# Kernel optimization log

Hardware: AMD Instinct MI355X
Metric: run time of the kernel (lower is better)

The kernel has to match this reference:

```python
import jax, jax.numpy as jnp
import numpy as np

D = 128          # state_dim
N_RBF = 20       # n radial basis functions
R_CUT = 10.0
N_NODES = 20000
N_EDGES = 320000
N_GRAPHS = 64
N_ATOMS = 10
ROUNDS = 2       # num_message_passing_rounds


def silu(x):
    return x * jax.nn.sigmoid(x)


def setup_inputs() -> dict:
    key = jax.random.key(0)
    ks = jax.random.split(key, 16)

    def p(k, shape, scale=None):
        scale = (1.0 / np.sqrt(shape[0])) if scale is None else scale
        return (jax.random.normal(k, shape, jnp.float32) * scale).astype(jnp.float32)

    return {
        "edge_src": jax.random.randint(ks[0], (N_EDGES,), 0, N_NODES, jnp.int32),
        "edge_dst": jax.random.randint(ks[1], (N_EDGES,), 0, N_NODES, jnp.int32),
        "edge_vec": jax.random.normal(ks[2], (N_EDGES, 3), jnp.float32) * 2.0,
        "atom_types": jax.random.randint(ks[3], (N_NODES,), 0, N_ATOMS, jnp.int32),
        "node_graph_index": jnp.sort(jax.random.randint(ks[4], (N_NODES,), 0, N_GRAPHS, jnp.int32)),
        "embedding": p(ks[5], (N_ATOMS, D), 1.0),
        "phi_w1": p(ks[6], (D, D)), "phi_b1": jnp.zeros((D,), jnp.float32),
        "phi_w2": p(ks[7], (D, 3 * D)), "phi_b2": jnp.zeros((3 * D,), jnp.float32),
        "filt_w": p(ks[8], (N_RBF, 3 * D)), "filt_b": jnp.zeros((3 * D,), jnp.float32),
        "upd_w1": p(ks[9], (2 * D, D)), "upd_b1": jnp.zeros((D,), jnp.float32),
        "upd_w2": p(ks[10], (D, 3 * D)), "upd_b2": jnp.zeros((3 * D,), jnp.float32),
        "U_w": p(ks[11], (D, D)), "V_w": p(ks[12], (D, D)),
        "out_w1": p(ks[13], (D, D)), "out_b1": jnp.zeros((D,), jnp.float32),
        "out_w2": p(ks[14], (D, 1)), "out_b2": jnp.zeros((1,), jnp.float32),
    }


def reference(edge_src, edge_dst, edge_vec, atom_types, node_graph_index,
              embedding, phi_w1, phi_b1, phi_w2, phi_b2, filt_w, filt_b,
              upd_w1, upd_b1, upd_w2, upd_b2, U_w, V_w,
              out_w1, out_b1, out_w2, out_b2):
    # init scalar states from atom-type embedding; vector states zero
    s = embedding[atom_types]                       # [N, D]
    v = jnp.zeros((N_NODES, 3, D), s.dtype)         # [N, 3, D]

    # geometry (constant across rounds)
    r = jnp.linalg.norm(edge_vec, axis=1)           # [E]
    k = jnp.arange(1, N_RBF + 1, dtype=s.dtype)
    rbf = jnp.sin(k[None, :] * jnp.pi * r[:, None] / R_CUT) / r[:, None]   # [E, n]
    fcut = 0.5 * (jnp.cos(jnp.pi * r / R_CUT) + 1.0) * (r < R_CUT)         # [E]
    W = (rbf @ filt_w + filt_b) * fcut[:, None]     # [E, 3D] filter * cosine cutoff
    dirs = edge_vec / r[:, None]                    # [E, 3] unit edge vectors

    for _ in range(ROUNDS):
        # ---- message block ----
        phi = silu(s[edge_src] @ phi_w1 + phi_b1) @ phi_w2 + phi_b2        # [E, 3D]
        m = phi * W
        m1, m2, m3 = m[:, :D], m[:, D:2 * D], m[:, 2 * D:]
        dv = v[edge_src] * m1[:, None, :] + dirs[:, :, None] * m3[:, None, :]  # [E, 3, D]
        s = s + jax.ops.segment_sum(m2, edge_dst, num_segments=N_NODES)
        v = v + jax.ops.segment_sum(dv, edge_dst, num_segments=N_NODES)

        # ---- update block ----
        U = v @ U_w                                  # [N, 3, D]
        Vp = v @ V_w                                 # [N, 3, D]
        UV = jnp.sum(U * Vp, axis=1)                 # [N, D]
        Vn = jnp.linalg.norm(Vp, axis=1)             # [N, D]
        a = silu(jnp.concatenate([Vn, s], axis=1) @ upd_w1 + upd_b1) @ upd_w2 + upd_b2  # [N, 3D]
        avv, asv, ass = a[:, :D], a[:, D:2 * D], a[:, 2 * D:]
        s = s + ass + UV * asv
        v = v + U * avv[:, None, :]

    # graph readout: index_add over node_graph_index, then output MLP
    g = jax.ops.segment_sum(s, node_graph_index, num_segments=N_GRAPHS)    # [G, D]
    return (silu(g @ out_w1 + out_b1) @ out_w2 + out_b2).reshape(-1)       # [G]
```

## Files before the change

### kernel.cpp

```cpp
#include <hip/hip_runtime.h>

#define NN 20000
#define NE 320000
#define NG 64
#define D 128
#define D3 384
#define NRBF 20
#define RBF_ROW 24
#define PI_F 3.14159265358979323846f
#define RCUT 10.0f

typedef unsigned int uint;
typedef unsigned short ushort;
typedef __attribute__((ext_vector_type(8))) short bf16x8;
typedef __attribute__((ext_vector_type(4))) float f32x4;

__device__ __forceinline__ float silu_f(float x) {
    return x / (1.0f + __expf(-x));
}
__device__ __forceinline__ float b2f(ushort u) {
    return __uint_as_float(((uint)u) << 16);
}
__device__ __forceinline__ ushort f2b(float f) {
    uint u = __float_as_uint(f);
    u = u + 0x7fffu + ((u >> 16) & 1u);
    return (ushort)(u >> 16);
}
__device__ __forceinline__ float plo(uint u) { return __uint_as_float(u << 16); }
__device__ __forceinline__ float phi_(uint u) { return __uint_as_float(u & 0xffff0000u); }

#define MFMA3(acc, aH, aL, bH, bL)                                          \
    acc = __builtin_amdgcn_mfma_f32_16x16x32_bf16(aL, bH, acc, 0, 0, 0);    \
    acc = __builtin_amdgcn_mfma_f32_16x16x32_bf16(aH, bL, acc, 0, 0, 0);    \
    acc = __builtin_amdgcn_mfma_f32_16x16x32_bf16(aH, bH, acc, 0, 0, 0);

__global__ __launch_bounds__(256) void mega_init(
    float* __restrict__ g, int* __restrict__ deg,
    const float* __restrict__ pw1, const float* __restrict__ pw2,
    ushort* __restrict__ w1th, ushort* __restrict__ w1tl,
    ushort* __restrict__ w2th, ushort* __restrict__ w2tl,
    const float* __restrict__ Uw, const float* __restrict__ Vw,
    const float* __restrict__ uw1, const float* __restrict__ uw2,
    ushort* __restrict__ uwt, ushort* __restrict__ vwt,
    ushort* __restrict__ u1t, ushort* __restrict__ u2t)
{
    int stride = gridDim.x * blockDim.x;
    int idx0 = blockIdx.x * blockDim.x + threadIdx.x;
    for (int i = idx0; i < NG * D; i += stride) g[i] = 0.f;
    for (int i = idx0; i < NN; i += stride) deg[i] = 0;
    for (int i = idx0; i < D * D; i += stride) {
        int j = i >> 7, k = i & 127;
        float x = pw1[k * D + j]; ushort h = f2b(x);
        w1th[i] = h; w1tl[i] = f2b(x - b2f(h));
        float a = Uw[k * D + j]; ushort ha = f2b(a);
        uwt[i] = ha; uwt[D * D + i] = f2b(a - b2f(ha));
        float b = Vw[k * D + j]; ushort hb = f2b(b);
        vwt[i] = hb; vwt[D * D + i] = f2b(b - b2f(hb));
    }
    for (int i = idx0; i < D3 * D; i += stride) {
        int j = i >> 7, k = i & 127;
        float x = pw2[k * D3 + j]; ushort h = f2b(x);
        w2th[i] = h; w2tl[i] = f2b(x - b2f(h));
        float y = uw2[k * D3 + j]; ushort hy = f2b(y);
        u2t[i] = hy; u2t[D3 * D + i] = f2b(y - b2f(hy));
    }
    for (int i = idx0; i < 2 * D * D; i += stride) {
        int j = i >> 8, k = i & 255;
        float x = uw1[k * D + j]; ushort h = f2b(x);
        u1t[i] = h; u1t[2 * D * D + i] = f2b(x - b2f(h));
    }
}

__global__ __launch_bounds__(256) void csr_count(
    const int* __restrict__ dst, int* __restrict__ deg)
{
    int e = blockIdx.x * blockDim.x + threadIdx.x;
    if (e < NE) atomicAdd(&deg[dst[e]], 1);
}

__global__ __launch_bounds__(1024) void scan_all(
    const int* __restrict__ deg, int* __restrict__ offs,
    int* __restrict__ cursor, int* __restrict__ bpos)
{
    __shared__ int part[1024];
    __shared__ int bc[64];
    int t = threadIdx.x;
    if (t < 64) bc[t] = 0;
    __syncthreads();
    const int per = (NN + 1023) / 1024;
    int base = t * per;
    int sum = 0;
    for (int i = 0; i < per; i++) {
        int idx = base + i;
        if (idx < NN) {
            int dg = deg[idx];
            sum += dg;
            int b = dg > 63 ? 63 : dg;
            atomicAdd(&bc[b], 1);
        }
    }
    part[t] = sum;
    __syncthreads();
    for (int off = 1; off < 1024; off <<= 1) {
        int vv = (t >= off) ? part[t - off] : 0;
        __syncthreads();
        part[t] += vv;
        __syncthreads();
    }
    int run = part[t] - sum;
    for (int i = 0; i < per; i++) {
        int idx = base + i;
        if (idx < NN) {
            offs[idx] = run;
            cursor[idx] = run;
            run += deg[idx];
        }
    }
    if (t == 1023) offs[NN] = run;
    __syncthreads();
    if (t == 0) {
        int r2 = 0;
        for (int b = 63; b >= 0; b--) { bpos[b] = r2; r2 += bc[b]; }
    }
}

__global__ __launch_bounds__(256) void scatter_all(
    const int* __restrict__ dst, int* __restrict__ cursor, int* __restrict__ eid,
    const int* __restrict__ deg, int* __restrict__ bpos, int* __restrict__ perm)
{
    int i = blockIdx.x * blockDim.x + threadIdx.x;
    if (i < NE) {
        int p = atomicAdd(&cursor[dst[i]], 1);
        eid[p] = i;
    }
    if (i < NN) {
        int b = deg[i]; if (b > 63) b = 63;
        int p = atomicAdd(&bpos[b], 1);
        perm[p] = i;
    }
}

__global__ __launch_bounds__(256) void edge_geom(
    const float* __restrict__ evec,
    float* __restrict__ rbf, float4* __restrict__ geo)
{
    int e = blockIdx.x * blockDim.x + threadIdx.x;
    if (e >= NE) return;
    float x = evec[e * 3 + 0], y = evec[e * 3 + 1], z = evec[e * 3 + 2];
    float r = sqrtf(x * x + y * y + z * z);
    float inv = 1.0f / r;
    float f = (r < RCUT) ? 0.5f * (cosf(PI_F * r / RCUT) + 1.0f) : 0.0f;
    float4 g;
    g.x = x * inv; g.y = y * inv; g.z = z * inv; g.w = f;
    geo[e] = g;
    float base = PI_F * r / RCUT;
    float sf = inv * f;
    #pragma unroll
    for (int k = 0; k < NRBF; k++) {
        rbf[(size_t)e * RBF_ROW + k] = sinf((float)(k + 1) * base) * sf;
    }
}

__global__ __launch_bounds__(128) void phi10(
    const float* __restrict__ emb,
    const float* __restrict__ w1, const float* __restrict__ b1,
    const float* __restrict__ w2, const float* __restrict__ b2,
    uint* __restrict__ ptab)
{
    __shared__ float el[D];
    __shared__ float hl[D];
    int t = blockIdx.x, j = threadIdx.x;
    el[j] = emb[t * D + j];
    __syncthreads();
    float acc = b1[j];
    for (int k = 0; k < D; k++) acc += el[k] * w1[k * D + j];
    hl[j] = silu_f(acc);
    __syncthreads();
    float a1 = b2[D + j], a2 = b2[2 * D + j];
    for (int k = 0; k < D; k++) {
        float h = hl[k];
        a1 += h * w2[k * D3 + D + j];
        a2 += h * w2[k * D3 + 2 * D + j];
    }
    ptab[t * D + j] = (uint)f2b(a1) | ((uint)f2b(a2) << 16);
}

__global__ __launch_bounds__(512)
__attribute__((amdgpu_waves_per_eu(4, 4)))
void node_gather_r0(
    const int* __restrict__ eid, const int* __restrict__ offs,
    const int* __restrict__ perm, const int* __restrict__ src,
    const int* __restrict__ atype, const float* __restrict__ emb,
    const uint* __restrict__ ptab,
    const float* __restrict__ rbf, const float4* __restrict__ geo,
    const float* __restrict__ filt_w, const float* __restrict__ filt_b,
    float* __restrict__ s_new, float* __restrict__ v_new)
{
    int wave = threadIdx.x >> 6;
    int lane = threadIdx.x & 63;
    int widx = blockIdx.x * 4 + (wave >> 1);
    if (widx >= NN) return;
    int node = __builtin_amdgcn_readfirstlane(perm[widx]);
    int half = wave & 1;
    int d = half * 64 + lane;

    float wr1[NRBF], wr2[NRBF];
    #pragma unroll
    for (int k = 0; k < NRBF; k++) {
        wr1[k] = filt_w[k * D3 + D + d];
        wr2[k] = filt_w[k * D3 + 2 * D + d];
    }
    float fb1 = filt_b[D + d], fb2 = filt_b[2 * D + d];
    int e0 = __builtin_amdgcn_readfirstlane(offs[node]);
    int e1 = __builtin_amdgcn_readfirstlane(offs[node + 1]);

    float acc_s = 0.f, av0 = 0.f, av1 = 0.f, av2 = 0.f;

    for (int i = e0; i < e1; i += 2) {
        bool hb = (i + 1 < e1);
        int ea = __builtin_amdgcn_readfirstlane(eid[i]);
        int eb = __builtin_amdgcn_readfirstlane(eid[hb ? i + 1 : i]);
        float mb = hb ? 1.0f : 0.0f;
        int sa = __builtin_amdgcn_readfirstlane(src[ea]);
        int sb = __builtin_amdgcn_readfirstlane(src[eb]);
        int ta = __builtin_amdgcn_readfirstlane(atype[sa]);
        int tb = __builtin_amdgcn_readfirstlane(atype[sb]);
        float4 ga = geo[ea];
        float4 gb = geo[eb];
        const float* rpa = rbf + (size_t)ea * RBF_ROW;
        const float* rpb = rbf + (size_t)eb * RBF_ROW;
        uint pka = ptab[ta * D + d];
        uint pkb = ptab[tb * D + d];

        float Wa1 = ga.w * fb1, Wa2 = ga.w * fb2;
        float Wb1 = gb.w * fb1, Wb2 = gb.w * fb2;
        #pragma unroll
        for (int k = 0; k < NRBF; k++) {
            float ra = rpa[k], rb = rpb[k];
            Wa1 += ra * wr1[k]; Wa2 += ra * wr2[k];
            Wb1 += rb * wr1[k]; Wb2 += rb * wr2[k];
        }
        float pa1 = plo(pka), pa2 = phi_(pka);
        float pb1 = plo(pkb), pb2 = phi_(pkb);

        float m2a = pa1 * Wa1, m3a = pa2 * Wa2;
        float m2b = pb1 * Wb1 * mb, m3b = pb2 * Wb2 * mb;
        acc_s += m2a + m2b;
        av0 += ga.x * m3a + gb.x * m3b;
        av1 += ga.y * m3a + gb.y * m3b;
        av2 += ga.z * m3a + gb.z * m3b;
    }

    int tn = __builtin_amdgcn_readfirstlane(atype[node]);
    s_new[node * D + d] = emb[tn * D + d] + acc_s;
    v_new[(node * 3 + 0) * D + d] = av0;
    v_new[(node * 3 + 1) * D + d] = av1;
    v_new[(node * 3 + 2) * D + d] = av2;
}

__global__ __launch_bounds__(512)
__attribute__((amdgpu_waves_per_eu(4, 4)))
void node_gather(
    const int* __restrict__ eid, const int* __restrict__ offs,
    const int* __restrict__ perm, const int* __restrict__ src,
    const ushort* __restrict__ pv,
    const float* __restrict__ s_old, const float* __restrict__ v_old,
    const float* __restrict__ rbf, const float4* __restrict__ geo,
    const float* __restrict__ filt_w, const float* __restrict__ filt_b,
    float* __restrict__ s_new, float* __restrict__ v_new)
{
    int wave = threadIdx.x >> 6;
    int lane = threadIdx.x & 63;
    int widx = blockIdx.x * 4 + (wave >> 1);
    if (widx >= NN) return;
    int node = __builtin_amdgcn_readfirstlane(perm[widx]);
    int half = wave & 1;
    int d = half * 64 + lane;

    float wr0[NRBF], wr1[NRBF], wr2[NRBF];
    #pragma unroll
    for (int k = 0; k < NRBF; k++) {
        wr0[k] = filt_w[k * D3 + d];
        wr1[k] = filt_w[k * D3 + D + d];
        wr2[k] = filt_w[k * D3 + 2 * D + d];
    }
    float fb0 = filt_b[d], fb1 = filt_b[D + d], fb2 = filt_b[2 * D + d];
    int e0 = __builtin_amdgcn_readfirstlane(offs[node]);
    int e1 = __builtin_amdgcn_readfirstlane(offs[node + 1]);

    float acc_s = 0.f, av0 = 0.f, av1 = 0.f, av2 = 0.f;
    size_t doff = (size_t)d * 6;

    for (int i = e0; i < e1; i += 2) {
        bool hb = (i + 1 < e1);
        int ea = __builtin_amdgcn_readfirstlane(eid[i]);
        int eb = __builtin_amdgcn_readfirstlane(eid[hb ? i + 1 : i]);
        float mb = hb ? 1.0f : 0.0f;
        int sa = __builtin_amdgcn_readfirstlane(src[ea]);
        int sb = __builtin_amdgcn_readfirstlane(src[eb]);
        float4 ga = geo[ea];
        float4 gb = geo[eb];
        const float* rpa = rbf + (size_t)ea * RBF_ROW;
        const float* rpb = rbf + (size_t)eb * RBF_ROW;
        uint3 pka = *(const uint3*)(pv + (size_t)sa * 768 + doff);
        uint3 pkb = *(const uint3*)(pv + (size_t)sb * 768 + doff);

        float Wa0 = ga.w * fb0, Wa1 = ga.w * fb1, Wa2 = ga.w * fb2;
        float Wb0 = gb.w * fb0, Wb1 = gb.w * fb1, Wb2 = gb.w * fb2;
        #pragma unroll
        for (int k = 0; k < NRBF; k++) {
            float ra = rpa[k], rb = rpb[k];
            Wa0 += ra * wr0[k]; Wa1 += ra * wr1[k]; Wa2 += ra * wr2[k];
            Wb0 += rb * wr0[k]; Wb1 += rb * wr1[k]; Wb2 += rb * wr2[k];
        }
        float pa0 = plo(pka.x), pa1 = phi_(pka.x), pa2 = plo(pka.y);
        float va0 = phi_(pka.y), va1 = plo(pka.z), va2 = phi_(pka.z);
        float pb0 = plo(pkb.x), pb1 = phi_(pkb.x), pb2 = plo(pkb.y);
        float vb0 = phi_(pkb.y), vb1 = plo(pkb.z), vb2 = phi_(pkb.z);

        float m1a = pa0 * Wa0, m2a = pa1 * Wa1, m3a = pa2 * Wa2;
        float m1b = pb0 * Wb0 * mb, m2b = pb1 * Wb1 * mb, m3b = pb2 * Wb2 * mb;
        acc_s += m2a + m2b;
        av0 += va0 * m1a + ga.x * m3a + vb0 * m1b + gb.x * m3b;
        av1 += va1 * m1a + ga.y * m3a + vb1 * m1b + gb.y * m3b;
        av2 += va2 * m1a + ga.z * m3a + vb2 * m1b + gb.z * m3b;
    }

    s_new[node * D + d] = s_old[node * D + d] + acc_s;
    v_new[(node * 3 + 0) * D + d] = v_old[(node * 3 + 0) * D + d] + av0;
    v_new[(node * 3 + 1) * D + d] = v_old[(node * 3 + 1) * D + d] + av1;
    v_new[(node * 3 + 2) * D + d] = v_old[(node * 3 + 2) * D + d] + av2;
}

template<bool FUSE>
__global__ __launch_bounds__(256) void node_vupd_mfma(
    float* __restrict__ s, float* __restrict__ v, ushort* __restrict__ pv,
    const ushort* __restrict__ uwt, const ushort* __restrict__ vwt,
    const ushort* __restrict__ u1t, const ushort* __restrict__ u2t,
    const float* __restrict__ ub1, const float* __restrict__ ub2,
    const ushort* __restrict__ w1th, const ushort* __restrict__ w1tl,
    const float* __restrict__ pb1,
    const ushort* __restrict__ w2th, const ushort* __restrict__ w2tl,
    const float* __restrict__ pb2)
{
    __shared__ __align__(16) char smem[47616];
    ushort* U_lds  = (ushort*)(smem);
    float*  UV_lds = (float*)(smem + 13056);
    ushort* a_hi   = (ushort*)(smem + 21504);
    ushort* a_lo   = a_hi + 48 * 136;
    ushort* x_hi   = (ushort*)(smem + 21504);
    ushort* x_lo   = x_hi + 16 * 264;
    ushort* h_hi   = x_lo + 16 * 264;
    ushort* h_lo   = h_hi + 16 * 136;
    float*  a_out  = (float*)(smem + 21504);

    int tid = threadIdx.x;
    int wave = tid >> 6, lane = tid & 63;
    int arow = lane & 15, kg = lane >> 4;
    int n0 = blockIdx.x * 16;

    #pragma unroll
    for (int it = 0; it < 6; it++) {
        int f4 = it * 256 + tid;
        int row = f4 >> 5;
        int c4 = (f4 & 31) * 4;
        int i = row >> 4, n = row & 15;
        float4 vv = *(const float4*)&v[((size_t)(n0 + n) * 3 + i) * D + c4];
        ushort h0 = f2b(vv.x), h1 = f2b(vv.y), h2 = f2b(vv.z), h3 = f2b(vv.w);
        ushort l0 = f2b(vv.x - b2f(h0)), l1 = f2b(vv.y - b2f(h1));
        ushort l2 = f2b(vv.z - b2f(h2)), l3 = f2b(vv.w - b2f(h3));
        uint2 ph; ph.x = (uint)h0 | ((uint)h1 << 16); ph.y = (uint)h2 | ((uint)h3 << 16);
        uint2 pl; pl.x = (uint)l0 | ((uint)l1 << 16); pl.y = (uint)l2 | ((uint)l3 << 16);
        *(uint2*)&a_hi[row * 136 + c4] = ph;
        *(uint2*)&a_lo[row * 136 + c4] = pl;
    }
    __syncthreads();

    f32x4 accU[3][2], accVp[3][2];
    #pragma unroll
    for (int i = 0; i < 3; i++)
        #pragma unroll
        for (int jtl = 0; jtl < 2; jtl++) {
            accU[i][jtl] = (f32x4){0.f, 0.f, 0.f, 0.f};
            accVp[i][jtl] = (f32x4){0.f, 0.f, 0.f, 0.f};
        }
    #pragma unroll
    for (int i = 0; i < 3; i++) {
        #pragma unroll
        for (int t = 0; t < 4; t++) {
            bf16x8 aH = *(const bf16x8*)&a_hi[(i * 16 + arow) * 136 + t * 32 + kg * 8];
            bf16x8 aL = *(const bf16x8*)&a_lo[(i * 16 + arow) * 136 + t * 32 + kg * 8];
            #pragma unroll
            for (int jtl = 0; jtl < 2; jtl++) {
                int j = (wave * 2 + jtl) * 16 + arow;
                bf16x8 bH = *(const bf16x8*)&uwt[(size_t)j * 128 + t * 32 + kg * 8];
                bf16x8 bL = *(const bf16x8*)&uwt[(size_t)D * D + (size_t)j * 128 + t * 32 + kg * 8];
                MFMA3(accU[i][jtl], aH, aL, bH, bL)
                bf16x8 cH = *(const bf16x8*)&vwt[(size_t)j * 128 + t * 32 + kg * 8];
                bf16x8 cL = *(const bf16x8*)&vwt[(size_t)D * D + (size_t)j * 128 + t * 32 + kg * 8];
                MFMA3(accVp[i][jtl], aH, aL, cH, cL)
            }
        }
    }
    __syncthreads();

    #pragma unroll
    for (int jtl = 0; jtl < 2; jtl++) {
        int jcol = (wave * 2 + jtl) * 16 + arow;
        #pragma unroll
        for (int r = 0; r < 4; r++) {
            int n = kg * 4 + r;
            #pragma unroll
            for (int i = 0; i < 3; i++)
                U_lds[(i * 16 + n) * 136 + jcol] = f2b(accU[i][jtl][r]);
            float uv = accU[0][jtl][r] * accVp[0][jtl][r]
                     + accU[1][jtl][r] * accVp[1][jtl][r]
                     + accU[2][jtl][r] * accVp[2][jtl][r];
            float nn = accVp[0][jtl][r] * accVp[0][jtl][r]
                     + accVp[1][jtl][r] * accVp[1][jtl][r]
                     + accVp[2][jtl][r] * accVp[2][jtl][r];
            UV_lds[n * 132 + jcol] = uv;
            float vn = sqrtf(nn);
            ushort hh = f2b(vn);
            x_hi[n * 264 + jcol] = hh;
            x_lo[n * 264 + jcol] = f2b(vn - b2f(hh));
        }
    }
    for (int it = 0; it < 8; it++) {
        int t8 = it * 256 + tid;
        int n = t8 >> 7, j = t8 & 127;
        float sv = s[(size_t)(n0 + n) * D + j];
        ushort hh = f2b(sv);
        x_hi[n * 264 + 128 + j] = hh;
        x_lo[n * 264 + 128 + j] = f2b(sv - b2f(hh));
    }
    __syncthreads();

    {
        f32x4 acc1[2];
        acc1[0] = (f32x4){0.f, 0.f, 0.f, 0.f};
        acc1[1] = (f32x4){0.f, 0.f, 0.f, 0.f};
        #pragma unroll
        for (int t = 0; t < 8; t++) {
            bf16x8 aH = *(const bf16x8*)&x_hi[arow * 264 + t * 32 + kg * 8];
            bf16x8 aL = *(const bf16x8*)&x_lo[arow * 264 + t * 32 + kg * 8];
            #pragma unroll
            for (int jtl = 0; jtl < 2; jtl++) {
                int j = (wave * 2 + jtl) * 16 + arow;
                bf16x8 bH = *(const bf16x8*)&u1t[(size_t)j * 256 + t * 32 + kg * 8];
                bf16x8 bL = *(const bf16x8*)&u1t[(size_t)2 * D * D + (size_t)j * 256 + t * 32 + kg * 8];
                MFMA3(acc1[jtl], aH, aL, bH, bL)
            }
        }
        #pragma unroll
        for (int jtl = 0; jtl < 2; jtl++) {
            int j = (wave * 2 + jtl) * 16 + arow;
            float bias = ub1[j];
            #pragma unroll
            for (int r = 0; r < 4; r++) {
                int n = kg * 4 + r;
                float hv = silu_f(acc1[jtl][r] + bias);
                ushort hh = f2b(hv);
                h_hi[n * 136 + j] = hh;
                h_lo[n * 136 + j] = f2b(hv - b2f(hh));
            }
        }
    }
    __syncthreads();

    f32x4 acc2[6];
    #pragma unroll
    for (int q = 0; q < 6; q++) acc2[q] = (f32x4){0.f, 0.f, 0.f, 0.f};
    #pragma unroll
    for (int t = 0; t < 4; t++) {
        bf16x8 aH = *(const bf16x8*)&h_hi[arow * 136 + t * 32 + kg * 8];
        bf16x8 aL = *(const bf16x8*)&h_lo[arow * 136 + t * 32 + kg * 8];
        #pragma unroll
        for (int q = 0; q < 6; q++) {
            int j = (wave * 6 + q) * 16 + arow;
            bf16x8 bH = *(const bf16x8*)&u2t[(size_t)j * 128 + t * 32 + kg * 8];
            bf16x8 bL = *(const bf16x8*)&u2t[(size_t)D3 * D + (size_t)j * 128 + t * 32 + kg * 8];
            MFMA3(acc2[q], aH, aL, bH, bL)
        }
    }
    __syncthreads();

    #pragma unroll
    for (int q = 0; q < 6; q++) {
        int j = (wave * 6 + q) * 16 + arow;
        float bias = ub2[j];
        #pragma unroll
        for (int r = 0; r < 4; r++)
            a_out[(kg * 4 + r) * 392 + j] = acc2[q][r] + bias;
    }
    __syncthreads();

    float snew_reg[8];
    #pragma unroll
    for (int it = 0; it < 8; it++) {
        int t8 = it * 256 + tid;
        int n = t8 >> 7, j = t8 & 127;
        float a0 = a_out[n * 392 + j];
        float a1 = a_out[n * 392 + 128 + j];
        float a2 = a_out[n * 392 + 256 + j];
        size_t sidx = (size_t)(n0 + n) * D + j;
        float snew = s[sidx] + a2 + UV_lds[n * 132 + j] * a1;
        s[sidx] = snew;
        snew_reg[it] = snew;
        float vf[3];
        #pragma unroll
        for (int i = 0; i < 3; i++) {
            size_t idx = ((size_t)(n0 + n) * 3 + i) * D + j;
            vf[i] = v[idx] + b2f(U_lds[(i * 16 + n) * 136 + j]) * a0;
            v[idx] = vf[i];
        }
        if (FUSE) {
            ushort* pvp = pv + ((size_t)(n0 + n) * 128 + j) * 6;
            pvp[3] = f2b(vf[0]);
            pvp[4] = f2b(vf[1]);
            pvp[5] = f2b(vf[2]);
        }
    }

    if (!FUSE) return;

    __syncthreads();
    #pragma unroll
    for (int it = 0; it < 8; it++) {
        int t8 = it * 256 + tid;
        int n = t8 >> 7, j = t8 & 127;
        float sv = snew_reg[it];
        ushort hh = f2b(sv);
        x_hi[n * 264 + j] = hh;
        x_lo[n * 264 + j] = f2b(sv - b2f(hh));
    }
    __syncthreads();

    {
        f32x4 accp[2];
        accp[0] = (f32x4){0.f, 0.f, 0.f, 0.f};
        accp[1] = (f32x4){0.f, 0.f, 0.f, 0.f};
        #pragma unroll
        for (int t = 0; t < 4; t++) {
            bf16x8 aH = *(const bf16x8*)&x_hi[arow * 264 + t * 32 + kg * 8];
            bf16x8 aL = *(const bf16x8*)&x_lo[arow * 264 + t * 32 + kg * 8];
            #pragma unroll
            for (int jtl = 0; jtl < 2; jtl++) {
                int j = (wave * 2 + jtl) * 16 + arow;
                bf16x8 bH = *(const bf16x8*)&w1th[(size_t)j * 128 + t * 32 + kg * 8];
                bf16x8 bL = *(const bf16x8*)&w1tl[(size_t)j * 128 + t * 32 + kg * 8];
                MFMA3(accp[jtl], aH, aL, bH, bL)
            }
        }
        __syncthreads();
        #pragma unroll
        for (int jtl = 0; jtl < 2; jtl++) {
            int j = (wave * 2 + jtl) * 16 + arow;
            float bias = pb1[j];
            #pragma unroll
            for (int r = 0; r < 4; r++) {
                int n = kg * 4 + r;
                float hv = silu_f(accp[jtl][r] + bias);
                ushort hh = f2b(hv);
                h_hi[n * 136 + j] = hh;
                h_lo[n * 136 + j] = f2b(hv - b2f(hh));
            }
        }
    }
    __syncthreads();

    {
        f32x4 accq[6];
        #pragma unroll
        for (int q = 0; q < 6; q++) accq[q] = (f32x4){0.f, 0.f, 0.f, 0.f};
        #pragma unroll
        for (int t = 0; t < 4; t++) {
            bf16x8 aH = *(const bf16x8*)&h_hi[arow * 136 + t * 32 + kg * 8];
            bf16x8 aL = *(const bf16x8*)&h_lo[arow * 136 + t * 32 + kg * 8];
            #pragma unroll
            for (int q = 0; q < 6; q++) {
                int j = (wave * 6 + q) * 16 + arow;
                bf16x8 bH = *(const bf16x8*)&w2th[(size_t)j * 128 + t * 32 + kg * 8];
                bf16x8 bL = *(const bf16x8*)&w2tl[(size_t)j * 128 + t * 32 + kg * 8];
                MFMA3(accq[q], aH, aL, bH, bL)
            }
        }
        #pragma unroll
        for (int q = 0; q < 6; q++) {
            int j = (wave * 6 + q) * 16 + arow;
            float bias = pb2[j];
            int seg = j >> 7;
            int ch  = j & 127;
            #pragma unroll
            for (int r = 0; r < 4; r++) {
                pv[((size_t)(n0 + kg * 4 + r) * 128 + ch) * 6 + seg] = f2b(accq[q][r] + bias);
            }
        }
    }
}

__global__ __launch_bounds__(128) void graph_sum(
    const float* __restrict__ s, const int* __restrict__ gi, float* __restrict__ g)
{
    int d = threadIdx.x;
    int n0 = blockIdx.x * 64;
    int n1 = n0 + 64; if (n1 > NN) n1 = NN;
    if (n0 >= NN) return;
    int cur = gi[n0];
    float acc = 0.0f;
    for (int n = n0; n < n1; n++) {
        int gn = gi[n];
        if (gn != cur) { atomicAdd(&g[cur * D + d], acc); acc = 0.0f; cur = gn; }
        acc += s[n * D + d];
    }
    atomicAdd(&g[cur * D + d], acc);
}

__global__ __launch_bounds__(128) void out_mlp(
    const float* __restrict__ g,
    const float* __restrict__ w1, const float* __restrict__ b1,
    const float* __restrict__ w2, const float* __restrict__ b2,
    float* __restrict__ out)
{
    __shared__ float gl[D];
    __shared__ float red[2];
    int j = threadIdx.x;
    int gr = blockIdx.x;
    gl[j] = g[gr * D + j];
    __syncthreads();
    float acc = b1[j];
    for (int k = 0; k < D; k++) acc += gl[k] * w1[k * D + j];
    float h = silu_f(acc) * w2[j];
    #pragma unroll
    for (int off = 32; off >= 1; off >>= 1) h += __shfl_down(h, off);
    if ((j & 63) == 0) red[j >> 6] = h;
    __syncthreads();
    if (j == 0) out[gr] = red[0] + red[1] + b2[0];
}

extern "C" void kernel_launch(void* const* d_in, const int* in_sizes, int n_in,
                              void* d_out, int out_size, void* d_ws, size_t ws_size,
                              hipStream_t stream)
{
    const int*   edge_src   = (const int*)  d_in[0];
    const int*   edge_dst   = (const int*)  d_in[1];
    const float* edge_vec   = (const float*)d_in[2];
    const int*   atom_types = (const int*)  d_in[3];
    const int*   node_gi    = (const int*)  d_in[4];
    const float* embedding  = (const float*)d_in[5];
    const float* phi_w1     = (const float*)d_in[6];
    const float* phi_b1     = (const float*)d_in[7];
    const float* phi_w2     = (const float*)d_in[8];
    const float* phi_b2     = (const float*)d_in[9];
    const float* filt_w     = (const float*)d_in[10];
    const float* filt_b     = (const float*)d_in[11];
    const float* upd_w1     = (const float*)d_in[12];
    const float* upd_b1     = (const float*)d_in[13];
    const float* upd_w2     = (const float*)d_in[14];
    const float* upd_b2     = (const float*)d_in[15];
    const float* U_w        = (const float*)d_in[16];
    const float* V_w        = (const float*)d_in[17];
    const float* out_w1     = (const float*)d_in[18];
    const float* out_b1     = (const float*)d_in[19];
    const float* out_w2     = (const float*)d_in[20];
    const float* out_b2     = (const float*)d_in[21];

    float* ws = (float*)d_ws;
    size_t o = 0;
    float* s_a   = ws + o; o += (size_t)NN * D;
    float* s_b   = ws + o; o += (size_t)NN * D;
    float* v_a   = ws + o; o += (size_t)NN * 3 * D;
    float* v_b   = ws + o; o += (size_t)NN * 3 * D;
    float* pv_f  = ws + o; o += (size_t)NN * 384;
    float* rbf_f = ws + o; o += (size_t)NE * RBF_ROW;
    float* geo   = ws + o; o += (size_t)NE * 4;
    float* g     = ws + o; o += (size_t)NG * D;
    float* w1t_f = ws + o; o += (size_t)D * D;
    float* w2t_f = ws + o; o += (size_t)D3 * D;
    float* uwt_f = ws + o; o += (size_t)D * D;
    float* vwt_f = ws + o; o += (size_t)D * D;
    float* u1t_f = ws + o; o += (size_t)2 * D * D;
    float* u2t_f = ws + o; o += (size_t)D3 * D;
    float* ptab_f= ws + o; o += (size_t)10 * D;
    int* deg     = (int*)(ws + o); o += NN;
    int* offs    = (int*)(ws + o); o += NN + 1;
    int* cursor  = (int*)(ws + o); o += NN;
    int* perm    = (int*)(ws + o); o += NN;
    int* bpos    = (int*)(ws + o); o += 64;
    int* eidb    = (int*)(ws + o); o += NE;

    ushort* pv    = (ushort*)pv_f;
    ushort* w1th  = (ushort*)w1t_f;
    ushort* w1tl  = w1th + (size_t)D * D;
    ushort* w2th  = (ushort*)w2t_f;
    ushort* w2tl  = w2th + (size_t)D3 * D;
    ushort* uwt   = (ushort*)uwt_f;
    ushort* vwt   = (ushort*)vwt_f;
    ushort* u1t   = (ushort*)u1t_f;
    ushort* u2t   = (ushort*)u2t_f;
    uint*   ptab  = (uint*)ptab_f;

    mega_init<<<512, 256, 0, stream>>>(g, deg, phi_w1, phi_w2,
                                       w1th, w1tl, w2th, w2tl,
                                       U_w, V_w, upd_w1, upd_w2,
                                       uwt, vwt, u1t, u2t);
    csr_count<<<(NE + 255) / 256, 256, 0, stream>>>(edge_dst, deg);
    scan_all<<<1, 1024, 0, stream>>>(deg, offs, cursor, bpos);
    scatter_all<<<(NE + 255) / 256, 256, 0, stream>>>(edge_dst, cursor, eidb,
                                                      deg, bpos, perm);
    edge_geom<<<(NE + 255) / 256, 256, 0, stream>>>(edge_vec, rbf_f, (float4*)geo);
    phi10<<<10, 128, 0, stream>>>(embedding, phi_w1, phi_b1, phi_w2, phi_b2, ptab);

    node_gather_r0<<<NN / 4, 512, 0, stream>>>(eidb, offs, perm, edge_src,
                                               atom_types, embedding, ptab,
                                               rbf_f, (const float4*)geo,
                                               filt_w, filt_b, s_b, v_b);
    node_vupd_mfma<true><<<NN / 16, 256, 0, stream>>>(s_b, v_b, pv,
                                                      uwt, vwt, u1t, u2t,
                                                      upd_b1, upd_b2,
                                                      w1th, w1tl, phi_b1,
                                                      w2th, w2tl, phi_b2);
    node_gather<<<NN / 4, 512, 0, stream>>>(eidb, offs, perm, edge_src, pv,
                                            s_b, v_b, rbf_f,
                                            (const float4*)geo, filt_w, filt_b,
                                            s_a, v_a);
    node_vupd_mfma<false><<<NN / 16, 256, 0, stream>>>(s_a, v_a, pv,
                                                       uwt, vwt, u1t, u2t,
                                                       upd_b1, upd_b2,
                                                       w1th, w1tl, phi_b1,
                                                       w2th, w2tl, phi_b2);

    graph_sum<<<(NN + 63) / 64, 128, 0, stream>>>(s_a, node_gi, g);
    out_mlp<<<NG, 128, 0, stream>>>(g, out_w1, out_b1, out_w2, out_b2, (float*)d_out);
}
```

Baseline: 663.4 us.

## Fuse degree count into edge_geom, graph readout into last update, keep U in registers

The edge-degree atomic count moves into the edge geometry kernel, and the separate graph_sum kernel is replaced by per-element atomicAdds into g inside the final node update. The node update now keeps U and UV in MFMA accumulator registers and writes outputs in the accumulator layout, no longer staging them through LDS. This cuts LDS use, which may raise occupancy. The final round also skips writing s and v back to global memory. The costs are many more global atomics on g, with 64 graphs contending, and less coalesced stores.

```diff
diff --git a/kernel.cpp b/kernel.cpp
--- a/kernel.cpp
+++ b/kernel.cpp
@@ -71,13 +71,6 @@
     }
 }
 
-__global__ __launch_bounds__(256) void csr_count(
-    const int* __restrict__ dst, int* __restrict__ deg)
-{
-    int e = blockIdx.x * blockDim.x + threadIdx.x;
-    if (e < NE) atomicAdd(&deg[dst[e]], 1);
-}
-
 __global__ __launch_bounds__(1024) void scan_all(
     const int* __restrict__ deg, int* __restrict__ offs,
     int* __restrict__ cursor, int* __restrict__ bpos)
@@ -140,12 +133,14 @@
     }
 }
 
-__global__ __launch_bounds__(256) void edge_geom(
-    const float* __restrict__ evec,
+__global__ __launch_bounds__(256) void edge_geom_count(
+    const float* __restrict__ evec, const int* __restrict__ dst,
+    int* __restrict__ deg,
     float* __restrict__ rbf, float4* __restrict__ geo)
 {
     int e = blockIdx.x * blockDim.x + threadIdx.x;
     if (e >= NE) return;
+    atomicAdd(&deg[dst[e]], 1);
     float x = evec[e * 3 + 0], y = evec[e * 3 + 1], z = evec[e * 3 + 2];
     float r = sqrtf(x * x + y * y + z * z);
     float inv = 1.0f / r;
@@ -335,6 +330,7 @@
 template<bool FUSE>
 __global__ __launch_bounds__(256) void node_vupd_mfma(
     float* __restrict__ s, float* __restrict__ v, ushort* __restrict__ pv,
+    const int* __restrict__ gi, float* __restrict__ g,
     const ushort* __restrict__ uwt, const ushort* __restrict__ vwt,
     const ushort* __restrict__ u1t, const ushort* __restrict__ u2t,
     const float* __restrict__ ub1, const float* __restrict__ ub2,
@@ -343,16 +339,14 @@
     const ushort* __restrict__ w2th, const ushort* __restrict__ w2tl,
     const float* __restrict__ pb2)
 {
-    __shared__ __align__(16) char smem[47616];
-    ushort* U_lds  = (ushort*)(smem);
-    float*  UV_lds = (float*)(smem + 13056);
-    ushort* a_hi   = (ushort*)(smem + 21504);
-    ushort* a_lo   = a_hi + 48 * 136;
-    ushort* x_hi   = (ushort*)(smem + 21504);
-    ushort* x_lo   = x_hi + 16 * 264;
-    ushort* h_hi   = x_lo + 16 * 264;
-    ushort* h_lo   = h_hi + 16 * 136;
-    float*  a_out  = (float*)(smem + 21504);
+    __shared__ __align__(16) char smem[26112];
+    ushort* a_hi = (ushort*)smem;
+    ushort* a_lo = a_hi + 48 * 136;
+    ushort* x_hi = (ushort*)smem;
+    ushort* x_lo = x_hi + 16 * 264;
+    ushort* h_hi = x_lo + 16 * 264;
+    ushort* h_lo = h_hi + 16 * 136;
+    float*  a_out = (float*)smem;
 
     int tid = threadIdx.x;
     int wave = tid >> 6, lane = tid & 63;
@@ -404,28 +398,27 @@
     }
     __syncthreads();
 
+    float uvr[2][4];
     #pragma unroll
     for (int jtl = 0; jtl < 2; jtl++) {
         int jcol = (wave * 2 + jtl) * 16 + arow;
         #pragma unroll
         for (int r = 0; r < 4; r++) {
             int n = kg * 4 + r;
-            #pragma unroll
-            for (int i = 0; i < 3; i++)
-                U_lds[(i * 16 + n) * 136 + jcol] = f2b(accU[i][jtl][r]);
             float uv = accU[0][jtl][r] * accVp[0][jtl][r]
                      + accU[1][jtl][r] * accVp[1][jtl][r]
                      + accU[2][jtl][r] * accVp[2][jtl][r];
             float nn = accVp[0][jtl][r] * accVp[0][jtl][r]
                      + accVp[1][jtl][r] * accVp[1][jtl][r]
                      + accVp[2][jtl][r] * accVp[2][jtl][r];
-            UV_lds[n * 132 + jcol] = uv;
+            uvr[jtl][r] = uv;
             float vn = sqrtf(nn);
             ushort hh = f2b(vn);
             x_hi[n * 264 + jcol] = hh;
             x_lo[n * 264 + jcol] = f2b(vn - b2f(hh));
         }
     }
+    #pragma unroll
     for (int it = 0; it < 8; it++) {
         int t8 = it * 256 + tid;
         int n = t8 >> 7, j = t8 & 127;
@@ -484,7 +477,6 @@
         }
     }
     __syncthreads();
-
     #pragma unroll
     for (int q = 0; q < 6; q++) {
         int j = (wave * 6 + q) * 16 + arow;
@@ -495,30 +487,33 @@
     }
     __syncthreads();
 
-    float snew_reg[8];
-    #pragma unroll
-    for (int it = 0; it < 8; it++) {
-        int t8 = it * 256 + tid;
-        int n = t8 >> 7, j = t8 & 127;
-        float a0 = a_out[n * 392 + j];
-        float a1 = a_out[n * 392 + 128 + j];
-        float a2 = a_out[n * 392 + 256 + j];
-        size_t sidx = (size_t)(n0 + n) * D + j;
-        float snew = s[sidx] + a2 + UV_lds[n * 132 + j] * a1;
-        s[sidx] = snew;
-        snew_reg[it] = snew;
-        float vf[3];
-        #pragma unroll
-        for (int i = 0; i < 3; i++) {
-            size_t idx = ((size_t)(n0 + n) * 3 + i) * D + j;
-            vf[i] = v[idx] + b2f(U_lds[(i * 16 + n) * 136 + j]) * a0;
-            v[idx] = vf[i];
-        }
-        if (FUSE) {
-            ushort* pvp = pv + ((size_t)(n0 + n) * 128 + j) * 6;
-            pvp[3] = f2b(vf[0]);
-            pvp[4] = f2b(vf[1]);
-            pvp[5] = f2b(vf[2]);
+    float snew_x[2][4];
+    #pragma unroll
+    for (int jtl = 0; jtl < 2; jtl++) {
+        int jcol = (wave * 2 + jtl) * 16 + arow;
+        #pragma unroll
+        for (int r = 0; r < 4; r++) {
+            int n = kg * 4 + r;
+            float a0 = a_out[n * 392 + jcol];
+            float a1 = a_out[n * 392 + 128 + jcol];
+            float a2 = a_out[n * 392 + 256 + jcol];
+            size_t sidx = (size_t)(n0 + n) * D + jcol;
+            float snew = s[sidx] + a2 + uvr[jtl][r] * a1;
+            if (FUSE) {
+                s[sidx] = snew;
+                snew_x[jtl][r] = snew;
+                ushort* pvp = pv + ((size_t)(n0 + n) * 128 + jcol) * 6;
+                #pragma unroll
+                for (int i = 0; i < 3; i++) {
+                    size_t idx = ((size_t)(n0 + n) * 3 + i) * D + jcol;
+                    float vf = v[idx] + accU[i][jtl][r] * a0;
+                    v[idx] = vf;
+                    pvp[3 + i] = f2b(vf);
+                }
+            } else {
+                int gn = gi[n0 + n];
+                atomicAdd(&g[(size_t)gn * D + jcol], snew);
+            }
         }
     }
 
@@ -526,13 +521,16 @@
 
     __syncthreads();
     #pragma unroll
-    for (int it = 0; it < 8; it++) {
-        int t8 = it * 256 + tid;
-        int n = t8 >> 7, j = t8 & 127;
-        float sv = snew_reg[it];
-        ushort hh = f2b(sv);
-        x_hi[n * 264 + j] = hh;
-        x_lo[n * 264 + j] = f2b(sv - b2f(hh));
+    for (int jtl = 0; jtl < 2; jtl++) {
+        int jcol = (wave * 2 + jtl) * 16 + arow;
+        #pragma unroll
+        for (int r = 0; r < 4; r++) {
+            int n = kg * 4 + r;
+            float sv = snew_x[jtl][r];
+            ushort hh = f2b(sv);
+            x_hi[n * 264 + jcol] = hh;
+            x_lo[n * 264 + jcol] = f2b(sv - b2f(hh));
+        }
     }
     __syncthreads();
 
@@ -597,23 +595,6 @@
             }
         }
     }
-}
-
-__global__ __launch_bounds__(128) void graph_sum(
-    const float* __restrict__ s, const int* __restrict__ gi, float* __restrict__ g)
-{
-    int d = threadIdx.x;
-    int n0 = blockIdx.x * 64;
-    int n1 = n0 + 64; if (n1 > NN) n1 = NN;
-    if (n0 >= NN) return;
-    int cur = gi[n0];
-    float acc = 0.0f;
-    for (int n = n0; n < n1; n++) {
-        int gn = gi[n];
-        if (gn != cur) { atomicAdd(&g[cur * D + d], acc); acc = 0.0f; cur = gn; }
-        acc += s[n * D + d];
-    }
-    atomicAdd(&g[cur * D + d], acc);
 }
 
 __global__ __launch_bounds__(128) void out_mlp(
@@ -704,18 +685,18 @@
                                        w1th, w1tl, w2th, w2tl,
                                        U_w, V_w, upd_w1, upd_w2,
                                        uwt, vwt, u1t, u2t);
-    csr_count<<<(NE + 255) / 256, 256, 0, stream>>>(edge_dst, deg);
+    edge_geom_count<<<(NE + 255) / 256, 256, 0, stream>>>(edge_vec, edge_dst, deg,
+                                                          rbf_f, (float4*)geo);
     scan_all<<<1, 1024, 0, stream>>>(deg, offs, cursor, bpos);
     scatter_all<<<(NE + 255) / 256, 256, 0, stream>>>(edge_dst, cursor, eidb,
                                                       deg, bpos, perm);
-    edge_geom<<<(NE + 255) / 256, 256, 0, stream>>>(edge_vec, rbf_f, (float4*)geo);
     phi10<<<10, 128, 0, stream>>>(embedding, phi_w1, phi_b1, phi_w2, phi_b2, ptab);
 
     node_gather_r0<<<NN / 4, 512, 0, stream>>>(eidb, offs, perm, edge_src,
                                                atom_types, embedding, ptab,
                                                rbf_f, (const float4*)geo,
                                                filt_w, filt_b, s_b, v_b);
-    node_vupd_mfma<true><<<NN / 16, 256, 0, stream>>>(s_b, v_b, pv,
+    node_vupd_mfma<true><<<NN / 16, 256, 0, stream>>>(s_b, v_b, pv, node_gi, g,
                                                       uwt, vwt, u1t, u2t,
                                                       upd_b1, upd_b2,
                                                       w1th, w1tl, phi_b1,
@@ -724,12 +705,11 @@
                                             s_b, v_b, rbf_f,
                                             (const float4*)geo, filt_w, filt_b,
                                             s_a, v_a);
-    node_vupd_mfma<false><<<NN / 16, 256, 0, stream>>>(s_a, v_a, pv,
+    node_vupd_mfma<false><<<NN / 16, 256, 0, stream>>>(s_a, v_a, pv, node_gi, g,
                                                        uwt, vwt, u1t, u2t,
                                                        upd_b1, upd_b2,
                                                        w1th, w1tl, phi_b1,
                                                        w2th, w2tl, phi_b2);
 
-    graph_sum<<<(NN + 63) / 64, 128, 0, stream>>>(s_a, node_gi, g);
     out_mlp<<<NG, 128, 0, stream>>>(g, out_w1, out_b1, out_w2, out_b2, (float*)d_out);
 }
```

New measurement: 699.2 us. 5.4% more time.

## Fuse degree count into edge geometry and graph readout into final update

Applied to the files above, without the earlier changes.

Merges the CSR degree-count atomics into the edge geometry kernel. It also removes the separate graph_sum kernel by having the last node update kernel atomically add each new scalar state into the per-graph sum. In the last round, the vector state update and the scalar store are skipped because nothing downstream reads them. The per-element atomics to only 64x128 targets can contend heavily, in exchange for fewer launches and less memory traffic.

```diff
diff --git a/kernel.cpp b/kernel.cpp
--- a/kernel.cpp
+++ b/kernel.cpp
@@ -71,13 +71,6 @@
     }
 }
 
-__global__ __launch_bounds__(256) void csr_count(
-    const int* __restrict__ dst, int* __restrict__ deg)
-{
-    int e = blockIdx.x * blockDim.x + threadIdx.x;
-    if (e < NE) atomicAdd(&deg[dst[e]], 1);
-}
-
 __global__ __launch_bounds__(1024) void scan_all(
     const int* __restrict__ deg, int* __restrict__ offs,
     int* __restrict__ cursor, int* __restrict__ bpos)
@@ -140,12 +133,14 @@
     }
 }
 
-__global__ __launch_bounds__(256) void edge_geom(
-    const float* __restrict__ evec,
+__global__ __launch_bounds__(256) void edge_geom_count(
+    const float* __restrict__ evec, const int* __restrict__ dst,
+    int* __restrict__ deg,
     float* __restrict__ rbf, float4* __restrict__ geo)
 {
     int e = blockIdx.x * blockDim.x + threadIdx.x;
     if (e >= NE) return;
+    atomicAdd(&deg[dst[e]], 1);
     float x = evec[e * 3 + 0], y = evec[e * 3 + 1], z = evec[e * 3 + 2];
     float r = sqrtf(x * x + y * y + z * z);
     float inv = 1.0f / r;
@@ -335,6 +330,7 @@
 template<bool FUSE>
 __global__ __launch_bounds__(256) void node_vupd_mfma(
     float* __restrict__ s, float* __restrict__ v, ushort* __restrict__ pv,
+    const int* __restrict__ gi, float* __restrict__ g,
     const ushort* __restrict__ uwt, const ushort* __restrict__ vwt,
     const ushort* __restrict__ u1t, const ushort* __restrict__ u2t,
     const float* __restrict__ ub1, const float* __restrict__ ub2,
@@ -410,9 +406,11 @@
         #pragma unroll
         for (int r = 0; r < 4; r++) {
             int n = kg * 4 + r;
-            #pragma unroll
-            for (int i = 0; i < 3; i++)
-                U_lds[(i * 16 + n) * 136 + jcol] = f2b(accU[i][jtl][r]);
+            if (FUSE) {
+                #pragma unroll
+                for (int i = 0; i < 3; i++)
+                    U_lds[(i * 16 + n) * 136 + jcol] = f2b(accU[i][jtl][r]);
+            }
             float uv = accU[0][jtl][r] * accVp[0][jtl][r]
                      + accU[1][jtl][r] * accVp[1][jtl][r]
                      + accU[2][jtl][r] * accVp[2][jtl][r];
@@ -500,25 +498,25 @@
     for (int it = 0; it < 8; it++) {
         int t8 = it * 256 + tid;
         int n = t8 >> 7, j = t8 & 127;
-        float a0 = a_out[n * 392 + j];
         float a1 = a_out[n * 392 + 128 + j];
         float a2 = a_out[n * 392 + 256 + j];
         size_t sidx = (size_t)(n0 + n) * D + j;
         float snew = s[sidx] + a2 + UV_lds[n * 132 + j] * a1;
-        s[sidx] = snew;
-        snew_reg[it] = snew;
-        float vf[3];
-        #pragma unroll
-        for (int i = 0; i < 3; i++) {
-            size_t idx = ((size_t)(n0 + n) * 3 + i) * D + j;
-            vf[i] = v[idx] + b2f(U_lds[(i * 16 + n) * 136 + j]) * a0;
-            v[idx] = vf[i];
-        }
         if (FUSE) {
+            float a0 = a_out[n * 392 + j];
+            s[sidx] = snew;
+            snew_reg[it] = snew;
             ushort* pvp = pv + ((size_t)(n0 + n) * 128 + j) * 6;
-            pvp[3] = f2b(vf[0]);
-            pvp[4] = f2b(vf[1]);
-            pvp[5] = f2b(vf[2]);
+            #pragma unroll
+            for (int i = 0; i < 3; i++) {
+                size_t idx = ((size_t)(n0 + n) * 3 + i) * D + j;
+                float vf = v[idx] + b2f(U_lds[(i * 16 + n) * 136 + j]) * a0;
+                v[idx] = vf;
+                pvp[3 + i] = f2b(vf);
+            }
+        } else {
+            int gn = gi[n0 + n];
+            atomicAdd(&g[(size_t)gn * D + j], snew);
         }
     }
 
@@ -597,23 +595,6 @@
             }
         }
     }
-}
-
-__global__ __launch_bounds__(128) void graph_sum(
-    const float* __restrict__ s, const int* __restrict__ gi, float* __restrict__ g)
-{
-    int d = threadIdx.x;
-    int n0 = blockIdx.x * 64;
-    int n1 = n0 + 64; if (n1 > NN) n1 = NN;
-    if (n0 >= NN) return;
-    int cur = gi[n0];
-    float acc = 0.0f;
-    for (int n = n0; n < n1; n++) {
-        int gn = gi[n];
-        if (gn != cur) { atomicAdd(&g[cur * D + d], acc); acc = 0.0f; cur = gn; }
-        acc += s[n * D + d];
-    }
-    atomicAdd(&g[cur * D + d], acc);
 }
 
 __global__ __launch_bounds__(128) void out_mlp(
@@ -704,18 +685,18 @@
                                        w1th, w1tl, w2th, w2tl,
                                        U_w, V_w, upd_w1, upd_w2,
                                        uwt, vwt, u1t, u2t);
-    csr_count<<<(NE + 255) / 256, 256, 0, stream>>>(edge_dst, deg);
+    edge_geom_count<<<(NE + 255) / 256, 256, 0, stream>>>(edge_vec, edge_dst, deg,
+                                                          rbf_f, (float4*)geo);
     scan_all<<<1, 1024, 0, stream>>>(deg, offs, cursor, bpos);
     scatter_all<<<(NE + 255) / 256, 256, 0, stream>>>(edge_dst, cursor, eidb,
                                                       deg, bpos, perm);
-    edge_geom<<<(NE + 255) / 256, 256, 0, stream>>>(edge_vec, rbf_f, (float4*)geo);
     phi10<<<10, 128, 0, stream>>>(embedding, phi_w1, phi_b1, phi_w2, phi_b2, ptab);
 
     node_gather_r0<<<NN / 4, 512, 0, stream>>>(eidb, offs, perm, edge_src,
                                                atom_types, embedding, ptab,
                                                rbf_f, (const float4*)geo,
                                                filt_w, filt_b, s_b, v_b);
-    node_vupd_mfma<true><<<NN / 16, 256, 0, stream>>>(s_b, v_b, pv,
+    node_vupd_mfma<true><<<NN / 16, 256, 0, stream>>>(s_b, v_b, pv, node_gi, g,
                                                       uwt, vwt, u1t, u2t,
                                                       upd_b1, upd_b2,
                                                       w1th, w1tl, phi_b1,
@@ -724,12 +705,11 @@
                                             s_b, v_b, rbf_f,
                                             (const float4*)geo, filt_w, filt_b,
                                             s_a, v_a);
-    node_vupd_mfma<false><<<NN / 16, 256, 0, stream>>>(s_a, v_a, pv,
+    node_vupd_mfma<false><<<NN / 16, 256, 0, stream>>>(s_a, v_a, pv, node_gi, g,
                                                        uwt, vwt, u1t, u2t,
                                                        upd_b1, upd_b2,
                                                        w1th, w1tl, phi_b1,
                                                        w2th, w2tl, phi_b2);
 
-    graph_sum<<<(NN + 63) / 64, 128, 0, stream>>>(s_a, node_gi, g);
     out_mlp<<<NG, 128, 0, stream>>>(g, out_w1, out_b1, out_w2, out_b2, (float*)d_out);
 }
```

Result: no change. 657.0 us (-1.0%).
